# Kernel optimization log

Measured on AMD Instinct MI355X. Metric: run time of the kernel, lower is better.

The kernel has to match this reference:

```python
import jax, jax.numpy as jnp
import numpy as np

N_NODES = 10000
N_EDGES = 320000
N_TYPES = 64
EDGE_INV = 8
MULT = 32          # env_embed_multiplicity
LAT = 256          # latent MLP width
SH_DIM = 9         # l = 0,1,2 -> 1+3+5
L_OFF = (0, 1, 4)
L_DIM = (1, 3, 5)
R_MAX = 6.0
POLY_P = 6.0
AVG_NEIGH = 32.0


def _w(key, fan_in, fan_out):
    return jax.random.normal(key, (fan_in, fan_out), jnp.float32) / np.sqrt(fan_in)


def setup_inputs() -> dict:
    key = jax.random.key(0)
    ks = jax.random.split(key, 20)
    return {
        "edge_attr": jax.random.normal(ks[0], (N_EDGES, SH_DIM), jnp.float32),
        "edge_length": jax.random.uniform(ks[1], (N_EDGES,), jnp.float32),
        "edge_invariants": jax.random.normal(ks[2], (N_EDGES, EDGE_INV), jnp.float32),
        "node_invariants": jax.random.uniform(ks[3], (N_NODES, N_TYPES), jnp.float32),
        "W2a": _w(ks[4], 2 * N_TYPES + EDGE_INV, LAT),
        "W2b": _w(ks[5], LAT, LAT),
        "Wl1a": _w(ks[6], LAT + MULT * 3, LAT),
        "Wl1b": _w(ks[7], LAT, LAT),
        "Wenv0": _w(ks[8], LAT, 2 * MULT * 3),
        "Wenv1": _w(ks[9], LAT, MULT * 3),
        "Wenvlin": jax.random.normal(ks[10], (2, 3, MULT, MULT), jnp.float32) / np.sqrt(MULT),
        "Wprod": jax.random.normal(ks[11], (2, 3, N_TYPES, MULT), jnp.float32) / np.sqrt(N_TYPES),
        "Wfeat": jax.random.normal(ks[12], (2, 3, MULT, MULT), jnp.float32) / np.sqrt(MULT),
        "Wfinlat": _w(ks[13], LAT, 3 * MULT * MULT),
        "Wro1": _w(ks[14], LAT + MULT * 3, LAT),
        "Wro2": _w(ks[15], LAT, 1),
        "edge_index": jax.random.randint(ks[16], (2, N_EDGES), 0, N_NODES),
    }


def poly_cutoff(x, p=POLY_P):
    # nequip polynomial cutoff, f(0)=1, f(1)=0 with p continuous derivatives
    f = (1.0 - (p + 1.0) * (p + 2.0) / 2.0 * x ** p
         + p * (p + 2.0) * x ** (p + 1.0)
         - p * (p + 1.0) / 2.0 * x ** (p + 2.0))
    return jnp.where(x < 1.0, f, 0.0)


def weight_channels(sh, w):
    # MakeWeightedChannels: sh [E,9], w [E,K,3 irreps] -> [E,K,9]
    return jnp.concatenate(
        [sh[:, None, o:o + d] * w[:, :, l:l + 1]
         for l, (o, d) in enumerate(zip(L_OFF, L_DIM))], axis=-1)


def mix_channels(x, W):
    # equivariant Linear: per-l channel mixing. x [N,K,9], W [3,K,K]
    return jnp.concatenate(
        [jnp.einsum('nkm,kj->njm', x[:, :, o:o + d], W[l])
         for l, (o, d) in enumerate(zip(L_OFF, L_DIM))], axis=-1)


def l_norms(x):
    # rotation-invariant per-(channel,l) norms: x [E,K,9] -> [E, K*3]
    return jnp.concatenate(
        [jnp.sqrt(jnp.sum(x[:, :, o:o + d] ** 2, axis=-1) + 1e-8)
         for (o, d) in zip(L_OFF, L_DIM)], axis=-1)


def _forward(edge_index, edge_attr, edge_length, edge_invariants, node_invariants,
             W2a, W2b, Wl1a, Wl1b, Wenv0, Wenv1, Wenvlin, Wprod, Wfeat,
             Wfinlat, Wro1, Wro2):
    center, neigh = edge_index[0], edge_index[1]
    n_nodes = node_invariants.shape[0]
    silu = jax.nn.silu
    cutoff = poly_cutoff(edge_length / R_MAX)                  # [E]
    alpha = jax.nn.sigmoid(0.0)                                # resnet update param init 0
    c_old = 1.0 / jnp.sqrt(alpha * alpha + 1.0)
    c_new = alpha * c_old
    norm = 1.0 / AVG_NEIGH                                     # env_sum_normalizations

    def env_and_product(env_w, lidx):
        # weighted SH channels -> scatter-sum env -> env linear -> product basis
        env_e = weight_channels(edge_attr, env_w) * cutoff[:, None, None]   # [E,K,9]
        env = jax.ops.segment_sum(env_e, center, num_segments=n_nodes) * norm
        env = mix_channels(env, Wenvlin[lidx])                  # [N,K,9]
        s = env[:, :, 0:1]                                      # scalar (l=0) channel
        ew = jnp.einsum('nt,ctk->nck', node_invariants, Wprod[lidx])  # element weights [N,3,K]
        prod = env * (ew[:, 0, :, None] + ew[:, 1, :, None] * s + ew[:, 2, :, None] * s * s)
        return mix_channels(prod, Wfeat[lidx])[center]          # gather back to edges [E,K,9]

    # ---- layer 0: two-body latent ----
    lat_in = jnp.concatenate(
        [node_invariants[center], node_invariants[neigh], edge_invariants], axis=-1)
    latents = cutoff[:, None] * silu(silu(lat_in @ W2a) @ W2b)  # [E,LAT]
    w_all = (latents @ Wenv0).reshape(-1, 2, MULT, 3)           # initial + env weights
    features0 = weight_channels(edge_attr, w_all[:, 0])         # initial weighted channels
    features = env_and_product(w_all[:, 1], 0)

    # ---- layer 1: latent resnet update ----
    lat_in = jnp.concatenate([latents, l_norms(features)], axis=-1)
    new_lat = silu(silu(lat_in @ Wl1a) @ Wl1b)
    latents = c_old * latents + c_new * cutoff[:, None] * new_lat
    features = env_and_product((latents @ Wenv1).reshape(-1, MULT, 3), 1)

    # ---- final per-edge linear (weights from latents) + diagonal 'uuu' TP -> invariants ----
    wfin = (latents @ Wfinlat).reshape(-1, 3, MULT, MULT)
    feat_fin = jnp.concatenate(
        [jnp.einsum('ekm,ekj->ejm', features[:, :, o:o + d], wfin[:, l])
         for l, (o, d) in enumerate(zip(L_OFF, L_DIM))], axis=-1)
    scal = jnp.concatenate(
        [jnp.sum(feat_fin[:, :, o:o + d] * features0[:, :, o:o + d], axis=-1)
         for (o, d) in zip(L_OFF, L_DIM)], axis=-1)              # [E, K*3]
    ro_in = jnp.concatenate([latents, scal], axis=-1)
    return silu(ro_in @ Wro1) @ Wro2                             # [E,1] edge energies


def reference(edge_attr, edge_length, edge_invariants, node_invariants,
              W2a, W2b, Wl1a, Wl1b, Wenv0, Wenv1, Wenvlin, Wprod, Wfeat,
              Wfinlat, Wro1, Wro2, edge_index):
    return _forward(edge_index, edge_attr, edge_length, edge_invariants, node_invariants,
                    W2a, W2b, Wl1a, Wl1b, Wenv0, Wenv1, Wenvlin, Wprod, Wfeat,
                    Wfinlat, Wro1, Wro2)
```

## Files before the change

### kernel.cpp

```cpp
#include <hip/hip_runtime.h>
#include <math.h>

#define NE 320000
#define NNODES 10000
#define EB 32
#define NBLK (NE / EB)
#define AST 360
#define BST 264
#define SST 98

typedef _Float16 f16x8 __attribute__((ext_vector_type(8)));
typedef float f32x4 __attribute__((ext_vector_type(4)));

__device__ __forceinline__ float silu(float x) { return x / (1.0f + __expf(-x)); }
__device__ __forceinline__ float cutf(float len) {
    float x = len * (1.0f / 6.0f);
    float x2 = x * x, x6 = x2 * x2 * x2;
    float f = 1.0f - 28.0f * x6 + 48.0f * x6 * x - 21.0f * x6 * x2;
    return (x < 1.0f) ? f : 0.0f;
}

__global__ __launch_bounds__(256) void k_zero(float* __restrict__ p, int n) {
    int i = blockIdx.x * 256 + threadIdx.x;
    if (i < n) p[i] = 0.f;
}

__global__ __launch_bounds__(256) void k_packf(const float* __restrict__ src,
                                               _Float16* __restrict__ dst,
                                               int K, int KS, int NT, int stride,
                                               int colOff) {
    int i = blockIdx.x * 256 + threadIdx.x;
    if (i >= NT * KS * 512) return;
    int j = i & 7, lane = (i >> 3) & 63;
    int blk = i >> 9;
    int ks = blk % KS, nt = blk / KS;
    int k = ks * 32 + (lane >> 4) * 8 + j;
    int n = colOff + nt * 16 + (lane & 15);
    dst[i] = (k < K) ? (_Float16)src[(size_t)k * stride + n] : (_Float16)0.f;
}

__global__ __launch_bounds__(256) void k_packfin4(const float* __restrict__ W,
                                                  _Float16* __restrict__ dst) {
    int i = blockIdx.x * 256 + threadIdx.x;
    int j = i & 7, lane = (i >> 3) & 63, u = (i >> 9) & 15, s = i >> 13;
    int nt = u >> 3, cc = u & 7;
    int l = s >> 5, ke = s & 31;
    int c = cc * 32 + ((lane >> 4) & 3) * 8 + j;
    int n = l * 1024 + ke * 32 + nt * 16 + (lane & 15);
    dst[i] = (_Float16)W[(size_t)c * 3072 + n];
}

template <int NT>
__device__ __forceinline__ void mfma_gemm2(int ksteps, const _Float16* Ah, int astride,
                                           const _Float16* __restrict__ Wt, int t,
                                           f32x4* acc0, f32x4* acc1) {
    int wave = t >> 6, lane = t & 63, r = lane & 15, g = lane >> 4;
    const int TPW = (NT + 3) / 4;
#pragma unroll
    for (int i = 0; i < TPW; ++i) {
        acc0[i] = (f32x4){0.f, 0.f, 0.f, 0.f};
        acc1[i] = (f32x4){0.f, 0.f, 0.f, 0.f};
    }
    for (int ks = 0; ks < ksteps; ++ks) {
        f16x8 a0 = *(const f16x8*)(Ah + r * astride + ks * 32 + g * 8);
        f16x8 a1 = *(const f16x8*)(Ah + (16 + r) * astride + ks * 32 + g * 8);
#pragma unroll
        for (int i = 0; i < TPW; ++i) {
            int nt = wave + 4 * i;
            if (nt < NT) {
                f16x8 b = *(const f16x8*)(Wt + ((size_t)(nt * ksteps + ks) * 64 + lane) * 8);
                acc0[i] = __builtin_amdgcn_mfma_f32_16x16x32_f16(a0, b, acc0[i], 0, 0, 0);
                acc1[i] = __builtin_amdgcn_mfma_f32_16x16x32_f16(a1, b, acc1[i], 0, 0, 0);
            }
        }
    }
}

__device__ __forceinline__ void gather_latin(
    const float* __restrict__ nodeinv, const float* __restrict__ edgeinv,
    const float* __restrict__ elen, const int* __restrict__ eidx,
    int e0, int t, _Float16* Ah, float* s_cut) {
    if (t < EB) s_cut[t] = cutf(elen[e0 + t]);
    for (int i = t; i < EB * 160; i += 256) {
        int ee = i / 160, k = i - ee * 160;
        int e = e0 + ee;
        float v;
        if (k < 64)       v = nodeinv[eidx[e] * 64 + k];
        else if (k < 128) v = nodeinv[eidx[NE + e] * 64 + (k - 64)];
        else if (k < 136) v = edgeinv[(size_t)e * 8 + (k - 128)];
        else              v = 0.f;
        Ah[ee * AST + k] = (_Float16)v;
    }
}

__device__ __forceinline__ void lat0_mfma2(const _Float16* __restrict__ W2aT,
                                           const _Float16* __restrict__ W2bT,
                                           int t, _Float16* Ah, _Float16* AhB,
                                           const float* s_cut) {
    int wave = t >> 6, lane = t & 63, r = lane & 15, g = lane >> 4;
    f32x4 acc0[4], acc1[4];
    mfma_gemm2<16>(5, Ah, AST, W2aT, t, acc0, acc1);
#pragma unroll
    for (int i = 0; i < 4; ++i) {
        int nt = wave + 4 * i;
#pragma unroll
        for (int i2 = 0; i2 < 4; ++i2) {
            AhB[(g * 4 + i2) * BST + nt * 16 + r] = (_Float16)silu(acc0[i][i2]);
            AhB[(16 + g * 4 + i2) * BST + nt * 16 + r] = (_Float16)silu(acc1[i][i2]);
        }
    }
    __syncthreads();
    mfma_gemm2<16>(8, AhB, BST, W2bT, t, acc0, acc1);
#pragma unroll
    for (int i = 0; i < 4; ++i) {
        int nt = wave + 4 * i;
#pragma unroll
        for (int i2 = 0; i2 < 4; ++i2) {
            int ro = g * 4 + i2, col = nt * 16 + r;
            Ah[ro * AST + col] = (_Float16)(s_cut[ro] * silu(acc0[i][i2]));
            Ah[(16 + ro) * AST + col] = (_Float16)(s_cut[16 + ro] * silu(acc1[i][i2]));
        }
    }
    __syncthreads();
}

__device__ __forceinline__ void gather_lnorm(const float* __restrict__ featN,
                                             const int* __restrict__ eidx,
                                             int e0, int t, _Float16* Ah) {
    for (int i = t; i < EB * 96; i += 256) {
        int ee = i / 96, rem = i - ee * 96;
        int l = rem >> 5, kk = rem & 31;
        int off = (l == 0) ? 0 : ((l == 1) ? 1 : 4);
        int d = (l == 0) ? 1 : ((l == 1) ? 3 : 5);
        const float* f = featN + (size_t)eidx[e0 + ee] * 288 + kk;
        float s = 1e-8f;
        for (int mm = off; mm < off + d; ++mm) { float x = f[mm * 32]; s = fmaf(x, x, s); }
        Ah[ee * AST + 256 + rem] = (_Float16)sqrtf(s);
    }
}

__device__ __forceinline__ void scatter_env(const float* __restrict__ edge_attr,
                                            const int* __restrict__ eidx,
                                            const float* s_w, const float* s_cut,
                                            int e0, int t, float* __restrict__ env) {
    for (int i = t; i < EB * 32; i += 256) {
        int el = i >> 5, k = i & 31;
        int e = e0 + el;
        float cw = s_cut[el];
        int n = eidx[e];
        float w0 = s_w[el * 96 + k * 3 + 0] * cw;
        float w1 = s_w[el * 96 + k * 3 + 1] * cw;
        float w2 = s_w[el * 96 + k * 3 + 2] * cw;
        float* dst = env + (size_t)n * 288 + k;
#pragma unroll
        for (int m = 0; m < 9; ++m) {
            float w = (m == 0) ? w0 : ((m < 4) ? w1 : w2);
            atomicAdd(dst + m * 32, edge_attr[(size_t)e * 9 + m] * w);
        }
    }
}

__device__ __forceinline__ void epi6_f32(const f32x4* acc0, const f32x4* acc1, int t,
                                         float* s_w) {
    int wave = t >> 6, lane = t & 63, r = lane & 15, g = lane >> 4;
#pragma unroll
    for (int i = 0; i < 2; ++i) {
        int nt = wave + 4 * i;
        if (nt < 6) {
#pragma unroll
            for (int i2 = 0; i2 < 4; ++i2) {
                s_w[(g * 4 + i2) * 96 + nt * 16 + r] = acc0[i][i2];
                s_w[(16 + g * 4 + i2) * 96 + nt * 16 + r] = acc1[i][i2];
            }
        }
    }
}

__global__ __launch_bounds__(256) void k1_lat_scatter0(
    const float* __restrict__ nodeinv, const float* __restrict__ edgeinv,
    const float* __restrict__ elen, const float* __restrict__ edge_attr,
    const int* __restrict__ eidx, const _Float16* __restrict__ W2aT,
    const _Float16* __restrict__ W2bT, const _Float16* __restrict__ Wenv0T,
    float* __restrict__ env, _Float16* __restrict__ lat0h,
    _Float16* __restrict__ w0h) {
    __shared__ alignas(16) _Float16 Ah[EB * AST];
    __shared__ alignas(16) _Float16 AhB[EB * BST];
    __shared__ float s_cut[EB];
    float* s_w = (float*)AhB;
    int t = threadIdx.x;
    int e0 = blockIdx.x * EB;
    int wave = t >> 6, lane = t & 63, r = lane & 15, g = lane >> 4;
    gather_latin(nodeinv, edgeinv, elen, eidx, e0, t, Ah, s_cut);
    __syncthreads();
    lat0_mfma2(W2aT, W2bT, t, Ah, AhB, s_cut);
    for (int i = t; i < EB * 32; i += 256) {
        int ee = i >> 5, c8 = (i & 31) * 8;
        *(f16x8*)(lat0h + (size_t)(e0 + ee) * 256 + c8) =
            *(const f16x8*)(Ah + ee * AST + c8);
    }
    f32x4 acc0[3], acc1[3];
    mfma_gemm2<12>(8, Ah, AST, Wenv0T, t, acc0, acc1);
#pragma unroll
    for (int i = 0; i < 3; ++i) {
        int nt = wave + 4 * i;
        if (nt < 6) {
#pragma unroll
            for (int i2 = 0; i2 < 4; ++i2) {
                w0h[(size_t)(e0 + g * 4 + i2) * 96 + nt * 16 + r] = (_Float16)acc0[i][i2];
                w0h[(size_t)(e0 + 16 + g * 4 + i2) * 96 + nt * 16 + r] = (_Float16)acc1[i][i2];
            }
        } else {
#pragma unroll
            for (int i2 = 0; i2 < 4; ++i2) {
                s_w[(g * 4 + i2) * 96 + (nt - 6) * 16 + r] = acc0[i][i2];
                s_w[(16 + g * 4 + i2) * 96 + (nt - 6) * 16 + r] = acc1[i][i2];
            }
        }
    }
    __syncthreads();
    scatter_env(edge_attr, eidx, s_w, s_cut, e0, t, env);
}

__global__ __launch_bounds__(288) void k_node(
    const float* envin, const float* __restrict__ nodeinv,
    const float* __restrict__ Wenvlin, const float* __restrict__ Wprod,
    const float* __restrict__ Wfeat, float* featOut) {
    __shared__ float s_env[288];
    __shared__ float s_inv[64];
    __shared__ float s_mix[288];
    __shared__ float s_ew[96];
    int n = blockIdx.x;
    int t = threadIdx.x;
    s_env[t] = envin[(size_t)n * 288 + t] * (1.0f / 32.0f);
    if (t < 64) s_inv[t] = nodeinv[n * 64 + t];
    __syncthreads();
    int m = t >> 5, j = t & 31;
    int l = (m == 0) ? 0 : ((m < 4) ? 1 : 2);
    float a = 0.f;
    for (int k = 0; k < 32; ++k) a = fmaf(s_env[m * 32 + k], Wenvlin[l * 1024 + k * 32 + j], a);
    if (t < 96) {
        int c = t >> 5, jj = t & 31;
        float b = 0.f;
        for (int tt = 0; tt < 64; ++tt) b = fmaf(s_inv[tt], Wprod[c * 2048 + tt * 32 + jj], b);
        s_ew[t] = b;
    }
    s_mix[t] = a;
    __syncthreads();
    float s = s_mix[j];
    float p = s_mix[t] * (s_ew[j] + s_ew[32 + j] * s + s_ew[64 + j] * s * s);
    __syncthreads();
    s_env[t] = p;
    __syncthreads();
    float o = 0.f;
    for (int jl = 0; jl < 32; ++jl) o = fmaf(s_env[m * 32 + jl], Wfeat[l * 1024 + jl * 32 + j], o);
    featOut[(size_t)n * 288 + t] = o;
}

__global__ __launch_bounds__(256) void k3_update_scatter1(
    const float* __restrict__ elen, const float* __restrict__ edge_attr,
    const int* __restrict__ eidx, const _Float16* __restrict__ Wl1aT,
    const _Float16* __restrict__ Wl1bT, const _Float16* __restrict__ Wenv1T,
    const float* __restrict__ featN0, float* __restrict__ env,
    _Float16* __restrict__ lat01h) {
    __shared__ alignas(16) _Float16 Ah[EB * AST];
    __shared__ alignas(16) _Float16 AhB[EB * BST];
    __shared__ float s_cut[EB];
    float* s_w = (float*)AhB;
    int t = threadIdx.x;
    int e0 = blockIdx.x * EB;
    int wave = t >> 6, lane = t & 63, r = lane & 15, g = lane >> 4;
    if (t < EB) s_cut[t] = cutf(elen[e0 + t]);
    for (int i = t; i < EB * 32; i += 256) {
        int ee = i >> 5, c8 = (i & 31) * 8;
        *(f16x8*)(Ah + ee * AST + c8) =
            *(const f16x8*)(lat01h + (size_t)(e0 + ee) * 256 + c8);
    }
    gather_lnorm(featN0, eidx, e0, t, Ah);
    __syncthreads();
    f32x4 acc0[4], acc1[4];
    mfma_gemm2<16>(11, Ah, AST, Wl1aT, t, acc0, acc1);
#pragma unroll
    for (int i = 0; i < 4; ++i) {
        int nt = wave + 4 * i;
#pragma unroll
        for (int i2 = 0; i2 < 4; ++i2) {
            AhB[(g * 4 + i2) * BST + nt * 16 + r] = (_Float16)silu(acc0[i][i2]);
            AhB[(16 + g * 4 + i2) * BST + nt * 16 + r] = (_Float16)silu(acc1[i][i2]);
        }
    }
    __syncthreads();
    mfma_gemm2<16>(8, AhB, BST, Wl1bT, t, acc0, acc1);
#pragma unroll
    for (int i = 0; i < 4; ++i) {
        int nt = wave + 4 * i;
#pragma unroll
        for (int i2 = 0; i2 < 4; ++i2) {
            int ro = g * 4 + i2, col = nt * 16 + r;
            float v0 = 0.8944271909999159f * (float)Ah[ro * AST + col] +
                       0.4472135954999579f * s_cut[ro] * silu(acc0[i][i2]);
            _Float16 h0 = (_Float16)v0;
            Ah[ro * AST + col] = h0;
            lat01h[(size_t)(e0 + ro) * 256 + col] = h0;
            float v1 = 0.8944271909999159f * (float)Ah[(16 + ro) * AST + col] +
                       0.4472135954999579f * s_cut[16 + ro] * silu(acc1[i][i2]);
            _Float16 h1 = (_Float16)v1;
            Ah[(16 + ro) * AST + col] = h1;
            lat01h[(size_t)(e0 + 16 + ro) * 256 + col] = h1;
        }
    }
    __syncthreads();
    mfma_gemm2<6>(8, Ah, AST, Wenv1T, t, acc0, acc1);
    epi6_f32(acc0, acc1, t, s_w);
    __syncthreads();
    scatter_env(edge_attr, eidx, s_w, s_cut, e0, t, env);
}

#define FEB 128
__global__ __launch_bounds__(512) void k5_fast(
    const float* __restrict__ edge_attr, const int* __restrict__ eidx,
    const _Float16* __restrict__ lat1h, const _Float16* __restrict__ w0h,
    const _Float16* __restrict__ BfinV4, const _Float16* __restrict__ Wro1T,
    const float* __restrict__ Wro2, const float* __restrict__ featN1,
    float* __restrict__ out) {
    __shared__ alignas(16) _Float16 Bst[2][8192];
    __shared__ alignas(16) _Float16 s_S[FEB * SST];
    __shared__ float s_ps[FEB][2];
    int t = threadIdx.x;
    int e0 = blockIdx.x * FEB;
    int wave = t >> 6, lane = t & 63;
    int r15 = lane & 15, g8 = lane >> 4;
    int prow = e0 + wave * 16 + r15;
    for (int i = t; i < FEB * 96; i += 512) {
        int ee = i / 96, rem = i - ee * 96;
        int l = rem >> 5, kk = rem & 31;
        int off = (l == 0) ? 0 : ((l == 1) ? 1 : 4);
        int d = (l == 0) ? 1 : ((l == 1) ? 3 : 5);
        int e = e0 + ee;
        const float* f = featN1 + (size_t)eidx[e] * 288 + kk;
        float s = 0.f;
        for (int mm = off; mm < off + d; ++mm)
            s = fmaf(f[mm * 32], edge_attr[(size_t)e * 9 + mm], s);
        s_S[ee * SST + rem] = (_Float16)s;
    }
    f16x8 a2[8];
#pragma unroll
    for (int cc = 0; cc < 8; ++cc)
        a2[cc] = *(const f16x8*)(lat1h + (size_t)prow * 256 + cc * 32 + g8 * 8);
    {
        const _Float16* g = BfinV4 + (size_t)t * 16;
        f16x8 g0 = *(const f16x8*)g, g1 = *(const f16x8*)(g + 8);
        *(f16x8*)&Bst[0][t * 16] = g0;
        *(f16x8*)&Bst[0][t * 16 + 8] = g1;
    }
    __syncthreads();
    f32x4 acc[3][2];
#pragma unroll
    for (int l = 0; l < 3; ++l)
#pragma unroll
        for (int nt = 0; nt < 2; ++nt) acc[l][nt] = (f32x4){0.f, 0.f, 0.f, 0.f};
    int cur = 0;
#pragma unroll
    for (int l = 0; l < 3; ++l) {
#pragma unroll 1
        for (int ke = 0; ke < 32; ++ke) {
            int s = l * 32 + ke;
            f16x8 g0, g1;
            if (s < 95) {
                const _Float16* g = BfinV4 + (size_t)(s + 1) * 8192 + t * 16;
                g0 = *(const f16x8*)g;
                g1 = *(const f16x8*)(g + 8);
            }
            _Float16 sh = s_S[(wave * 16 + r15) * SST + l * 32 + ke];
            f16x8 sb = {sh, sh, sh, sh, sh, sh, sh, sh};
#pragma unroll
            for (int nt = 0; nt < 2; ++nt) {
#pragma unroll
                for (int cc = 0; cc < 8; ++cc) {
                    f16x8 b = *(const f16x8*)&Bst[cur][(nt * 8 + cc) * 512 + lane * 8];
                    f16x8 ap = a2[cc] * sb;
                    acc[l][nt] = __builtin_amdgcn_mfma_f32_16x16x32_f16(ap, b, acc[l][nt], 0, 0, 0);
                }
            }
            __syncthreads();
            if (s < 95) {
                *(f16x8*)&Bst[cur ^ 1][t * 16] = g0;
                *(f16x8*)&Bst[cur ^ 1][t * 16 + 8] = g1;
            }
            __syncthreads();
            cur ^= 1;
        }
    }
#pragma unroll
    for (int l = 0; l < 3; ++l) {
#pragma unroll
        for (int nt = 0; nt < 2; ++nt) {
#pragma unroll
            for (int i2 = 0; i2 < 4; ++i2) {
                int row = g8 * 4 + i2;
                int jo = nt * 16 + r15;
                float w0 = (float)w0h[(size_t)(e0 + wave * 16 + row) * 96 + jo * 3 + l];
                s_S[(wave * 16 + row) * SST + l * 32 + jo] =
                    (_Float16)(acc[l][nt][i2] * w0);
            }
        }
    }
    __syncthreads();
    int mh2 = wave >> 1, w2 = wave & 1;
    f32x4 racc[8][2];
#pragma unroll
    for (int i = 0; i < 8; ++i)
#pragma unroll
        for (int mt2 = 0; mt2 < 2; ++mt2) racc[i][mt2] = (f32x4){0.f, 0.f, 0.f, 0.f};
#pragma unroll
    for (int ks = 0; ks < 11; ++ks) {
        f16x8 af0, af1;
        if (ks < 8) {
            af0 = *(const f16x8*)(lat1h + (size_t)(e0 + mh2 * 32 + r15) * 256 + ks * 32 + g8 * 8);
            af1 = *(const f16x8*)(lat1h + (size_t)(e0 + mh2 * 32 + 16 + r15) * 256 + ks * 32 + g8 * 8);
        } else {
            af0 = *(const f16x8*)(s_S + (mh2 * 32 + r15) * SST + (ks - 8) * 32 + g8 * 8);
            af1 = *(const f16x8*)(s_S + (mh2 * 32 + 16 + r15) * SST + (ks - 8) * 32 + g8 * 8);
        }
#pragma unroll
        for (int i = 0; i < 8; ++i) {
            int nt = w2 + 2 * i;
            f16x8 b = *(const f16x8*)(Wro1T + ((size_t)(nt * 11 + ks) * 64 + lane) * 8);
            racc[i][0] = __builtin_amdgcn_mfma_f32_16x16x32_f16(af0, b, racc[i][0], 0, 0, 0);
            racc[i][1] = __builtin_amdgcn_mfma_f32_16x16x32_f16(af1, b, racc[i][1], 0, 0, 0);
        }
    }
    float v[2][4];
#pragma unroll
    for (int mt2 = 0; mt2 < 2; ++mt2)
#pragma unroll
        for (int i2 = 0; i2 < 4; ++i2) v[mt2][i2] = 0.f;
#pragma unroll
    for (int i = 0; i < 8; ++i) {
        int col = (w2 + 2 * i) * 16 + r15;
        float w2f = Wro2[col];
#pragma unroll
        for (int mt2 = 0; mt2 < 2; ++mt2)
#pragma unroll
            for (int i2 = 0; i2 < 4; ++i2) v[mt2][i2] += silu(racc[i][mt2][i2]) * w2f;
    }
#pragma unroll
    for (int off = 1; off < 16; off <<= 1)
#pragma unroll
        for (int mt2 = 0; mt2 < 2; ++mt2)
#pragma unroll
            for (int i2 = 0; i2 < 4; ++i2) v[mt2][i2] += __shfl_xor(v[mt2][i2], off);
    if (r15 == 0) {
#pragma unroll
        for (int mt2 = 0; mt2 < 2; ++mt2)
#pragma unroll
            for (int i2 = 0; i2 < 4; ++i2)
                s_ps[mh2 * 32 + mt2 * 16 + g8 * 4 + i2][w2] = v[mt2][i2];
    }
    __syncthreads();
    if (t < FEB) out[e0 + t] = s_ps[t][0] + s_ps[t][1];
}

extern "C" void kernel_launch(void* const* d_in, const int* in_sizes, int n_in,
                              void* d_out, int out_size, void* d_ws, size_t ws_size,
                              hipStream_t stream) {
    (void)in_sizes; (void)n_in; (void)out_size;
    const float* edge_attr = (const float*)d_in[0];
    const float* edge_len  = (const float*)d_in[1];
    const float* edge_inv  = (const float*)d_in[2];
    const float* node_inv  = (const float*)d_in[3];
    const float* W2a     = (const float*)d_in[4];
    const float* W2b     = (const float*)d_in[5];
    const float* Wl1a    = (const float*)d_in[6];
    const float* Wl1b    = (const float*)d_in[7];
    const float* Wenv0   = (const float*)d_in[8];
    const float* Wenv1   = (const float*)d_in[9];
    const float* Wenvlin = (const float*)d_in[10];
    const float* Wprod   = (const float*)d_in[11];
    const float* Wfeat   = (const float*)d_in[12];
    const float* Wfinlat = (const float*)d_in[13];
    const float* Wro1    = (const float*)d_in[14];
    const float* Wro2    = (const float*)d_in[15];
    const int* eidx      = (const int*)d_in[16];
    float* out = (float*)d_out;

    _Float16* p = (_Float16*)d_ws;
    _Float16* BfinV4  = p; p += 786432;
    _Float16* W2aT    = p; p += 40960;
    _Float16* W2bT    = p; p += 65536;
    _Float16* Wenv0T  = p; p += 49152;
    _Float16* Wenv1T  = p; p += 24576;
    _Float16* Wl1aT   = p; p += 90112;
    _Float16* Wl1bT   = p; p += 65536;
    _Float16* Wro1T   = p; p += 90112;
    float* env    = (float*)p;
    float* featN0 = env + (size_t)NNODES * 288;
    char* after = (char*)(featN0 + (size_t)NNODES * 288);
    size_t need_base = (size_t)(after - (char*)d_ws);
    if (ws_size < need_base) return;
    _Float16* lat01h = (_Float16*)after;
    _Float16* w0h    = lat01h + (size_t)NE * 256;
    size_t need = need_base + (size_t)NE * (256 + 96) * sizeof(_Float16);
    if (ws_size < need) return;

    const int ENV_N = NNODES * 288;
    k_packfin4<<<3072, 256, 0, stream>>>(Wfinlat, BfinV4);
    k_packf<<<160, 256, 0, stream>>>(W2a, W2aT, 136, 5, 16, 256, 0);
    k_packf<<<256, 256, 0, stream>>>(W2b, W2bT, 256, 8, 16, 256, 0);
    k_packf<<<192, 256, 0, stream>>>(Wenv0, Wenv0T, 256, 8, 12, 192, 0);
    k_packf<<<96, 256, 0, stream>>>(Wenv1, Wenv1T, 256, 8, 6, 96, 0);
    k_packf<<<352, 256, 0, stream>>>(Wl1a, Wl1aT, 352, 11, 16, 256, 0);
    k_packf<<<256, 256, 0, stream>>>(Wl1b, Wl1bT, 256, 8, 16, 256, 0);
    k_packf<<<352, 256, 0, stream>>>(Wro1, Wro1T, 352, 11, 16, 256, 0);

    k_zero<<<(ENV_N + 255) / 256, 256, 0, stream>>>(env, ENV_N);
    k1_lat_scatter0<<<NBLK, 256, 0, stream>>>(node_inv, edge_inv, edge_len, edge_attr,
                                              eidx, W2aT, W2bT, Wenv0T, env, lat01h, w0h);
    k_node<<<NNODES, 288, 0, stream>>>(env, node_inv, Wenvlin, Wprod, Wfeat, featN0);
    k_zero<<<(ENV_N + 255) / 256, 256, 0, stream>>>(env, ENV_N);
    k3_update_scatter1<<<NBLK, 256, 0, stream>>>(edge_len, edge_attr, eidx,
                                                 Wl1aT, Wl1bT, Wenv1T, featN0, env, lat01h);
    k_node<<<NNODES, 288, 0, stream>>>(env, node_inv, Wenvlin + 3072, Wprod + 6144,
                                       Wfeat + 3072, env);
    k5_fast<<<NE / FEB, 512, 0, stream>>>(edge_attr, eidx, lat01h, w0h, BfinV4, Wro1T,
                                          Wro2, env, out);
}
```

Measured before the change: 2.926 ms.

## Switch final edge kernel to 32x32x16 MFMA with 4 waves of 32 rows

Rewrites the final per-edge kernel to use 32x32x16 f16 MFMA instructions. Each of 4 waves now owns 32 edges instead of 8 waves owning 16. Wfinlat and Wro1 are repacked into matching layouts, one redundant barrier per k-step is dropped, and the readout reduction writes straight to the output without a shared-memory partial-sum buffer. The aim is more arithmetic per LDS B-fragment load and less synchronisation. In exchange each wave holds more registers (16 A fragments plus 32-wide accumulators), which may lower occupancy.

```diff
diff --git a/kernel.cpp b/kernel.cpp
--- a/kernel.cpp
+++ b/kernel.cpp
@@ -11,6 +11,7 @@
 
 typedef _Float16 f16x8 __attribute__((ext_vector_type(8)));
 typedef float f32x4 __attribute__((ext_vector_type(4)));
+typedef float f32x16 __attribute__((ext_vector_type(16)));
 
 __device__ __forceinline__ float silu(float x) { return x / (1.0f + __expf(-x)); }
 __device__ __forceinline__ float cutf(float len) {
@@ -39,15 +40,25 @@
     dst[i] = (k < K) ? (_Float16)src[(size_t)k * stride + n] : (_Float16)0.f;
 }
 
-__global__ __launch_bounds__(256) void k_packfin4(const float* __restrict__ W,
+__global__ __launch_bounds__(256) void k_packfin3(const float* __restrict__ W,
                                                   _Float16* __restrict__ dst) {
     int i = blockIdx.x * 256 + threadIdx.x;
-    int j = i & 7, lane = (i >> 3) & 63, u = (i >> 9) & 15, s = i >> 13;
-    int nt = u >> 3, cc = u & 7;
+    int j = i & 7, lane = (i >> 3) & 63, q = (i >> 9) & 15, s = i >> 13;
     int l = s >> 5, ke = s & 31;
-    int c = cc * 32 + ((lane >> 4) & 3) * 8 + j;
-    int n = l * 1024 + ke * 32 + nt * 16 + (lane & 15);
+    int c = q * 16 + (lane >> 5) * 8 + j;
+    int n = l * 1024 + ke * 32 + (lane & 31);
     dst[i] = (_Float16)W[(size_t)c * 3072 + n];
+}
+
+__global__ __launch_bounds__(256) void k_packro5(const float* __restrict__ W,
+                                                 _Float16* __restrict__ dst) {
+    int i = blockIdx.x * 256 + threadIdx.x;
+    if (i >= 90112) return;
+    int j = i & 7, lane = (i >> 3) & 63, u = i >> 9;
+    int cb = u / 22, ks2 = u - cb * 22;
+    int k = ks2 * 16 + (lane >> 5) * 8 + j;
+    int n = cb * 32 + (lane & 31);
+    dst[i] = (_Float16)W[(size_t)k * 256 + n];
 }
 
 template <int NT>
@@ -316,21 +327,19 @@
 }
 
 #define FEB 128
-__global__ __launch_bounds__(512) void k5_fast(
+__global__ __launch_bounds__(256) void k5_fast(
     const float* __restrict__ edge_attr, const int* __restrict__ eidx,
     const _Float16* __restrict__ lat1h, const _Float16* __restrict__ w0h,
-    const _Float16* __restrict__ BfinV4, const _Float16* __restrict__ Wro1T,
+    const _Float16* __restrict__ Bfin3, const _Float16* __restrict__ Wro1T32,
     const float* __restrict__ Wro2, const float* __restrict__ featN1,
     float* __restrict__ out) {
     __shared__ alignas(16) _Float16 Bst[2][8192];
     __shared__ alignas(16) _Float16 s_S[FEB * SST];
-    __shared__ float s_ps[FEB][2];
     int t = threadIdx.x;
     int e0 = blockIdx.x * FEB;
     int wave = t >> 6, lane = t & 63;
-    int r15 = lane & 15, g8 = lane >> 4;
-    int prow = e0 + wave * 16 + r15;
-    for (int i = t; i < FEB * 96; i += 512) {
+    int r31 = lane & 31, kh5 = lane >> 5;
+    for (int i = t; i < FEB * 96; i += 256) {
         int ee = i / 96, rem = i - ee * 96;
         int l = rem >> 5, kk = rem & 31;
         int off = (l == 0) ? 0 : ((l == 1) ? 1 : 4);
@@ -342,49 +351,49 @@
             s = fmaf(f[mm * 32], edge_attr[(size_t)e * 9 + mm], s);
         s_S[ee * SST + rem] = (_Float16)s;
     }
-    f16x8 a2[8];
-#pragma unroll
-    for (int cc = 0; cc < 8; ++cc)
-        a2[cc] = *(const f16x8*)(lat1h + (size_t)prow * 256 + cc * 32 + g8 * 8);
-    {
-        const _Float16* g = BfinV4 + (size_t)t * 16;
-        f16x8 g0 = *(const f16x8*)g, g1 = *(const f16x8*)(g + 8);
-        *(f16x8*)&Bst[0][t * 16] = g0;
-        *(f16x8*)&Bst[0][t * 16 + 8] = g1;
-    }
-    __syncthreads();
-    f32x4 acc[3][2];
-#pragma unroll
-    for (int l = 0; l < 3; ++l)
-#pragma unroll
-        for (int nt = 0; nt < 2; ++nt) acc[l][nt] = (f32x4){0.f, 0.f, 0.f, 0.f};
+    f16x8 a2[16];
+#pragma unroll
+    for (int q = 0; q < 16; ++q)
+        a2[q] = *(const f16x8*)(lat1h + (size_t)(e0 + wave * 32 + r31) * 256 +
+                                q * 16 + kh5 * 8);
+#pragma unroll
+    for (int c = 0; c < 4; ++c) {
+        f16x8 gc = *(const f16x8*)(Bfin3 + (size_t)(c * 256 + t) * 8);
+        *(f16x8*)&Bst[0][(c * 256 + t) * 8] = gc;
+    }
+    __syncthreads();
+    const f32x16 z16 = {0.f, 0.f, 0.f, 0.f, 0.f, 0.f, 0.f, 0.f,
+                        0.f, 0.f, 0.f, 0.f, 0.f, 0.f, 0.f, 0.f};
+    f32x16 acc[3];
+#pragma unroll
+    for (int l = 0; l < 3; ++l) acc[l] = z16;
     int cur = 0;
 #pragma unroll
     for (int l = 0; l < 3; ++l) {
 #pragma unroll 1
         for (int ke = 0; ke < 32; ++ke) {
             int s = l * 32 + ke;
-            f16x8 g0, g1;
+            f16x8 g0, g1, g2, g3;
             if (s < 95) {
-                const _Float16* g = BfinV4 + (size_t)(s + 1) * 8192 + t * 16;
-                g0 = *(const f16x8*)g;
-                g1 = *(const f16x8*)(g + 8);
-            }
-            _Float16 sh = s_S[(wave * 16 + r15) * SST + l * 32 + ke];
+                const _Float16* g = Bfin3 + (size_t)(s + 1) * 8192;
+                g0 = *(const f16x8*)(g + (size_t)(0 * 256 + t) * 8);
+                g1 = *(const f16x8*)(g + (size_t)(1 * 256 + t) * 8);
+                g2 = *(const f16x8*)(g + (size_t)(2 * 256 + t) * 8);
+                g3 = *(const f16x8*)(g + (size_t)(3 * 256 + t) * 8);
+            }
+            _Float16 sh = s_S[(wave * 32 + r31) * SST + l * 32 + ke];
             f16x8 sb = {sh, sh, sh, sh, sh, sh, sh, sh};
 #pragma unroll
-            for (int nt = 0; nt < 2; ++nt) {
-#pragma unroll
-                for (int cc = 0; cc < 8; ++cc) {
-                    f16x8 b = *(const f16x8*)&Bst[cur][(nt * 8 + cc) * 512 + lane * 8];
-                    f16x8 ap = a2[cc] * sb;
-                    acc[l][nt] = __builtin_amdgcn_mfma_f32_16x16x32_f16(ap, b, acc[l][nt], 0, 0, 0);
-                }
-            }
-            __syncthreads();
+            for (int q = 0; q < 16; ++q) {
+                f16x8 b = *(const f16x8*)&Bst[cur][q * 512 + lane * 8];
+                f16x8 ap = a2[q] * sb;
+                acc[l] = __builtin_amdgcn_mfma_f32_32x32x16_f16(ap, b, acc[l], 0, 0, 0);
+            }
             if (s < 95) {
-                *(f16x8*)&Bst[cur ^ 1][t * 16] = g0;
-                *(f16x8*)&Bst[cur ^ 1][t * 16 + 8] = g1;
+                *(f16x8*)&Bst[cur ^ 1][(0 * 256 + t) * 8] = g0;
+                *(f16x8*)&Bst[cur ^ 1][(1 * 256 + t) * 8] = g1;
+                *(f16x8*)&Bst[cur ^ 1][(2 * 256 + t) * 8] = g2;
+                *(f16x8*)&Bst[cur ^ 1][(3 * 256 + t) * 8] = g3;
             }
             __syncthreads();
             cur ^= 1;
@@ -393,71 +402,43 @@
 #pragma unroll
     for (int l = 0; l < 3; ++l) {
 #pragma unroll
-        for (int nt = 0; nt < 2; ++nt) {
-#pragma unroll
-            for (int i2 = 0; i2 < 4; ++i2) {
-                int row = g8 * 4 + i2;
-                int jo = nt * 16 + r15;
-                float w0 = (float)w0h[(size_t)(e0 + wave * 16 + row) * 96 + jo * 3 + l];
-                s_S[(wave * 16 + row) * SST + l * 32 + jo] =
-                    (_Float16)(acc[l][nt][i2] * w0);
-            }
-        }
-    }
-    __syncthreads();
-    int mh2 = wave >> 1, w2 = wave & 1;
-    f32x4 racc[8][2];
-#pragma unroll
-    for (int i = 0; i < 8; ++i)
-#pragma unroll
-        for (int mt2 = 0; mt2 < 2; ++mt2) racc[i][mt2] = (f32x4){0.f, 0.f, 0.f, 0.f};
-#pragma unroll
-    for (int ks = 0; ks < 11; ++ks) {
-        f16x8 af0, af1;
-        if (ks < 8) {
-            af0 = *(const f16x8*)(lat1h + (size_t)(e0 + mh2 * 32 + r15) * 256 + ks * 32 + g8 * 8);
-            af1 = *(const f16x8*)(lat1h + (size_t)(e0 + mh2 * 32 + 16 + r15) * 256 + ks * 32 + g8 * 8);
-        } else {
-            af0 = *(const f16x8*)(s_S + (mh2 * 32 + r15) * SST + (ks - 8) * 32 + g8 * 8);
-            af1 = *(const f16x8*)(s_S + (mh2 * 32 + 16 + r15) * SST + (ks - 8) * 32 + g8 * 8);
-        }
-#pragma unroll
-        for (int i = 0; i < 8; ++i) {
-            int nt = w2 + 2 * i;
-            f16x8 b = *(const f16x8*)(Wro1T + ((size_t)(nt * 11 + ks) * 64 + lane) * 8);
-            racc[i][0] = __builtin_amdgcn_mfma_f32_16x16x32_f16(af0, b, racc[i][0], 0, 0, 0);
-            racc[i][1] = __builtin_amdgcn_mfma_f32_16x16x32_f16(af1, b, racc[i][1], 0, 0, 0);
-        }
-    }
-    float v[2][4];
-#pragma unroll
-    for (int mt2 = 0; mt2 < 2; ++mt2)
-#pragma unroll
-        for (int i2 = 0; i2 < 4; ++i2) v[mt2][i2] = 0.f;
-#pragma unroll
-    for (int i = 0; i < 8; ++i) {
-        int col = (w2 + 2 * i) * 16 + r15;
-        float w2f = Wro2[col];
-#pragma unroll
-        for (int mt2 = 0; mt2 < 2; ++mt2)
-#pragma unroll
-            for (int i2 = 0; i2 < 4; ++i2) v[mt2][i2] += silu(racc[i][mt2][i2]) * w2f;
-    }
-#pragma unroll
-    for (int off = 1; off < 16; off <<= 1)
-#pragma unroll
-        for (int mt2 = 0; mt2 < 2; ++mt2)
-#pragma unroll
-            for (int i2 = 0; i2 < 4; ++i2) v[mt2][i2] += __shfl_xor(v[mt2][i2], off);
-    if (r15 == 0) {
-#pragma unroll
-        for (int mt2 = 0; mt2 < 2; ++mt2)
-#pragma unroll
-            for (int i2 = 0; i2 < 4; ++i2)
-                s_ps[mh2 * 32 + mt2 * 16 + g8 * 4 + i2][w2] = v[mt2][i2];
-    }
-    __syncthreads();
-    if (t < FEB) out[e0 + t] = s_ps[t][0] + s_ps[t][1];
+        for (int reg = 0; reg < 16; ++reg) {
+            int row = (reg & 3) + 8 * (reg >> 2) + 4 * kh5;
+            int jo = r31;
+            float w0 = (float)w0h[(size_t)(e0 + wave * 32 + row) * 96 + jo * 3 + l];
+            s_S[(wave * 32 + row) * SST + l * 32 + jo] = (_Float16)(acc[l][reg] * w0);
+        }
+    }
+    __syncthreads();
+    float v16[16];
+#pragma unroll
+    for (int reg = 0; reg < 16; ++reg) v16[reg] = 0.f;
+#pragma unroll 1
+    for (int cb = 0; cb < 8; ++cb) {
+        f32x16 racc = z16;
+#pragma unroll
+        for (int ks2 = 0; ks2 < 22; ++ks2) {
+            f16x8 af = (ks2 < 16)
+                ? a2[ks2]
+                : *(const f16x8*)&s_S[(wave * 32 + r31) * SST + (ks2 - 16) * 16 + kh5 * 8];
+            f16x8 b = *(const f16x8*)(Wro1T32 + ((size_t)(cb * 22 + ks2) * 512 + lane * 8));
+            racc = __builtin_amdgcn_mfma_f32_32x32x16_f16(af, b, racc, 0, 0, 0);
+        }
+        float w2 = Wro2[cb * 32 + r31];
+#pragma unroll
+        for (int reg = 0; reg < 16; ++reg) v16[reg] += silu(racc[reg]) * w2;
+    }
+#pragma unroll
+    for (int off = 1; off < 32; off <<= 1)
+#pragma unroll
+        for (int reg = 0; reg < 16; ++reg) v16[reg] += __shfl_xor(v16[reg], off);
+    if (r31 == 0) {
+#pragma unroll
+        for (int reg = 0; reg < 16; ++reg) {
+            int row = (reg & 3) + 8 * (reg >> 2) + 4 * kh5;
+            out[e0 + wave * 32 + row] = v16[reg];
+        }
+    }
 }
 
 extern "C" void kernel_launch(void* const* d_in, const int* in_sizes, int n_in,
@@ -484,14 +465,14 @@
     float* out = (float*)d_out;
 
     _Float16* p = (_Float16*)d_ws;
-    _Float16* BfinV4  = p; p += 786432;
+    _Float16* Bfin3   = p; p += 786432;
     _Float16* W2aT    = p; p += 40960;
     _Float16* W2bT    = p; p += 65536;
     _Float16* Wenv0T  = p; p += 49152;
     _Float16* Wenv1T  = p; p += 24576;
     _Float16* Wl1aT   = p; p += 90112;
     _Float16* Wl1bT   = p; p += 65536;
-    _Float16* Wro1T   = p; p += 90112;
+    _Float16* Wro1T32 = p; p += 90112;
     float* env    = (float*)p;
     float* featN0 = env + (size_t)NNODES * 288;
     char* after = (char*)(featN0 + (size_t)NNODES * 288);
@@ -503,14 +484,14 @@
     if (ws_size < need) return;
 
     const int ENV_N = NNODES * 288;
-    k_packfin4<<<3072, 256, 0, stream>>>(Wfinlat, BfinV4);
+    k_packfin3<<<3072, 256, 0, stream>>>(Wfinlat, Bfin3);
     k_packf<<<160, 256, 0, stream>>>(W2a, W2aT, 136, 5, 16, 256, 0);
     k_packf<<<256, 256, 0, stream>>>(W2b, W2bT, 256, 8, 16, 256, 0);
     k_packf<<<192, 256, 0, stream>>>(Wenv0, Wenv0T, 256, 8, 12, 192, 0);
     k_packf<<<96, 256, 0, stream>>>(Wenv1, Wenv1T, 256, 8, 6, 96, 0);
     k_packf<<<352, 256, 0, stream>>>(Wl1a, Wl1aT, 352, 11, 16, 256, 0);
     k_packf<<<256, 256, 0, stream>>>(Wl1b, Wl1bT, 256, 8, 16, 256, 0);
-    k_packf<<<352, 256, 0, stream>>>(Wro1, Wro1T, 352, 11, 16, 256, 0);
+    k_packro5<<<352, 256, 0, stream>>>(Wro1, Wro1T32);
 
     k_zero<<<(ENV_N + 255) / 256, 256, 0, stream>>>(env, ENV_N);
     k1_lat_scatter0<<<NBLK, 256, 0, stream>>>(node_inv, edge_inv, edge_len, edge_attr,
@@ -521,6 +502,6 @@
                                                  Wl1aT, Wl1bT, Wenv1T, featN0, env, lat01h);
     k_node<<<NNODES, 288, 0, stream>>>(env, node_inv, Wenvlin + 3072, Wprod + 6144,
                                        Wfeat + 3072, env);
-    k5_fast<<<NE / FEB, 512, 0, stream>>>(edge_attr, eidx, lat01h, w0h, BfinV4, Wro1T,
+    k5_fast<<<NE / FEB, 256, 0, stream>>>(edge_attr, eidx, lat01h, w0h, Bfin3, Wro1T32,
                                           Wro2, env, out);
 }
```

After: 2.684 ms. 1.09x faster.
